# Kernel tuning notes

Measured on AMD Instinct MI355X. Metric: run time of the kernel, lower is better.

## Reference

```python
import jax, jax.numpy as jnp
import numpy as np

GH, GW, H, B, IN = 4, 2, 512, 8192, 1
FC_HID = H // 2
NC = GH * GW
BN_EPS = 1e-5


def setup_inputs() -> dict:
    key = jax.random.key(0)
    ks = jax.random.split(key, 20)
    def n(k, shape, s=1.0):
        return jax.random.normal(k, shape, dtype=jnp.float32) * s
    return {
        "x": n(ks[0], (B, GH, GW)),
        "h_ext": n(ks[1], (B, H), 0.1),
        "c_ext": n(ks[2], (B, H), 0.1),
        "grid_h": n(ks[3], (GH, GW, B, H), 0.1),
        "grid_c": n(ks[4], (GH, GW, B, H), 0.1),
        "Wh": n(ks[5], (NC, H, 3 * H), (3 * H) ** -0.5),
        "bh": n(ks[6], (NC, H), 0.01),
        "Wc": n(ks[7], (NC, H, 3 * H), (3 * H) ** -0.5),
        "bc": n(ks[8], (NC, H), 0.01),
        "W_ih": n(ks[9], (NC, 4 * H, IN), 1.0),
        "W_hh": n(ks[10], (NC, 4 * H, H), H ** -0.5),
        "b_ih": n(ks[11], (NC, 4 * H), 0.01),
        "b_hh": n(ks[12], (NC, 4 * H), 0.01),
        "W1": n(ks[13], (FC_HID, 2 * H), (2 * H) ** -0.5),
        "b1": n(ks[14], (FC_HID,), 0.01),
        "W2": n(ks[15], (1, FC_HID), FC_HID ** -0.5),
        "b2": n(ks[16], (1,), 0.01),
        "gamma": jnp.ones((1,), jnp.float32),
        "beta": jnp.zeros((1,), jnp.float32),
    }


def _lattice_forward(x, h_ext, c_ext, grid_h, grid_c, Wh, bh, Wc, bc,
                     W_ih, W_hh, b_ih, b_hh, W1, b1, W2, b2, gamma, beta):
    b = x.shape[0]
    zeros = jnp.zeros((b, H), x.dtype)
    # python lists over the small fixed 4x2 grid (strict left/up dependency)
    sh = [[grid_h[i, j] for j in range(GW)] for i in range(GH)]
    sc = [[grid_c[i, j] for j in range(GW)] for i in range(GH)]
    for i in range(GH):
        for j in range(GW):
            k = i * GW + j
            h_prev, c_prev = sh[i][j], sc[i][j]
            if i == 0 and j == 0:
                h_left, c_left = h_ext, c_ext
            elif j > 0:
                h_left, c_left = sh[i][j - 1], sc[i][j - 1]
            else:
                h_left, c_left = zeros, zeros
            if i > 0:
                h_up, c_up = sh[i - 1][j], sc[i - 1][j]
            else:
                h_up, c_up = zeros, zeros
            comb_h = jnp.concatenate([h_left, h_up, h_prev], axis=1)  # [B,3H]
            comb_c = jnp.concatenate([c_left, c_up, c_prev], axis=1)
            ph = comb_h @ Wh[k].T + bh[k]  # [B,H]
            pc = comb_c @ Wc[k].T + bc[k]
            xi = x[:, i, j][:, None]  # [B,1]
            gates = xi @ W_ih[k].T + b_ih[k] + ph @ W_hh[k].T + b_hh[k]  # [B,4H]
            ig, fg, gg, og = jnp.split(gates, 4, axis=1)
            c_new = jax.nn.sigmoid(fg) * pc + jax.nn.sigmoid(ig) * jnp.tanh(gg)
            h_new = jax.nn.sigmoid(og) * jnp.tanh(c_new)
            sh[i][j], sc[i][j] = h_new, c_new
    final_h = sh[-1][-1] + h_ext
    final_c = sc[-1][-1] + c_ext
    final = jnp.concatenate([final_h, final_c], axis=1)  # [B,2H]
    hid = jax.nn.relu(final @ W1.T + b1)
    out = hid @ W2.T + b2  # [B,1]
    # BatchNorm1d in training mode: biased batch stats over the batch dim
    mu = jnp.mean(out, axis=0, keepdims=True)
    var = jnp.mean((out - mu) ** 2, axis=0, keepdims=True)
    out = gamma * (out - mu) * jax.lax.rsqrt(var + BN_EPS) + beta
    out = jax.nn.sigmoid(out)
    new_gh = jnp.stack([jnp.stack(row) for row in sh])  # [GH,GW,B,H]
    new_gc = jnp.stack([jnp.stack(row) for row in sc])
    return out, final_h, final_c, new_gh, new_gc


def reference(x, h_ext, c_ext, grid_h, grid_c, Wh, bh, Wc, bc,
              W_ih, W_hh, b_ih, b_hh, W1, b1, W2, b2, gamma, beta):
    return _lattice_forward(x, h_ext, c_ext, grid_h, grid_c, Wh, bh, Wc, bc,
                            W_ih, W_hh, b_ih, b_hh, W1, b1, W2, b2, gamma, beta)
```

## Files before the change

kernel.cpp:

```cpp
#include <hip/hip_runtime.h>
#include <stdint.h>

#define B_SZ 8192
#define H_SZ 512
static const size_t BH = (size_t)B_SZ * H_SZ;

typedef short bfrag8 __attribute__((ext_vector_type(8)));
typedef float f32x4 __attribute__((ext_vector_type(4)));

__device__ __forceinline__ unsigned short f2bf(float f) {
  union { float f; uint32_t u; } c; c.f = f;
  uint32_t u = c.u;
  uint32_t r = (u + 0x7FFFu + ((u >> 16) & 1u)) >> 16;
  return (unsigned short)r;
}
__device__ __forceinline__ float bf2f(unsigned short u) {
  union { uint32_t u; float f; } c; c.u = ((uint32_t)u) << 16;
  return c.f;
}
__device__ __forceinline__ float sigm(float x) { return 1.0f / (1.0f + __expf(-x)); }
__device__ __forceinline__ float tanh_fast(float x) {
  float cx = fminf(fmaxf(x, -15.0f), 15.0f);
  float e = __expf(2.0f * cx);
  return (e - 1.0f) / (e + 1.0f);
}

__device__ __forceinline__ void gload16(const void* g, void* l) {
  __builtin_amdgcn_global_load_lds(
      (const __attribute__((address_space(1))) void*)g,
      (__attribute__((address_space(3))) void*)l, 16, 0, 0);
}

__device__ __forceinline__ void xcd_swizzle(int& bx, int& by, int& bz) {
  int nx = gridDim.x, ny = gridDim.y, nz = gridDim.z;
  int nwg = nx * ny * nz;
  int id = blockIdx.x + nx * (blockIdx.y + ny * blockIdx.z);
  int q = nwg >> 3, r = nwg & 7;
  int xcd = id & 7, lin = id >> 3;
  int swz = (xcd < r ? xcd * (q + 1) : r * (q + 1) + (xcd - r) * q) + lin;
  bx = swz % nx; swz /= nx;
  by = swz % ny; bz = swz / ny;
}

struct PJob {
  const unsigned short* A[3];
  int co[3];
  int nseg, relu;
  const unsigned short* B;
  const float* bias;
  unsigned short* outBf;
};
struct PArgs {
  PJob j[8];
  int ldA, ldB, outStride;
};

__global__ __launch_bounds__(256, 2) void pgemm_k(PArgs pa) {
  __shared__ __align__(16) char lds[65536];
  int bx, by, bz;
  xcd_swizzle(bx, by, bz);
  const PJob jb = pa.j[bz];
  const int tid = threadIdx.x;
  const int lane = tid & 63;
  const int wv = tid >> 6;
  const int wr = wv >> 1, wc = wv & 1;
  const int m0 = by * 128;
  const int ldA = pa.ldA;

  int rowA[4], cg[4];
  const char* browPtr[4];
#pragma unroll
  for (int q = 0; q < 4; ++q) {
    int cl = q * 256 + tid;
    int row = cl >> 3, cs = cl & 7;
    cg[q] = cs ^ (row & 7);
    rowA[q] = row;
    browPtr[q] = (const char*)jb.B + (size_t)(bx * 128 + row) * pa.ldB * 2;
  }

  f32x4 acc[4][4];
#pragma unroll
  for (int a = 0; a < 4; ++a)
#pragma unroll
    for (int b = 0; b < 4; ++b) acc[a][b] = f32x4{0.f, 0.f, 0.f, 0.f};

  const int nt = jb.nseg * 8;

  auto stagef = [&](int t, int buf) {
    int s = t >> 3, k0 = (t & 7) << 6;
    const char* Abase = (const char*)jb.A[s];
    int coB = jb.co[s] * 2;
    char* base = lds + buf * 32768;
#pragma unroll
    for (int q = 0; q < 4; ++q)
      gload16(Abase + ((size_t)(m0 + rowA[q]) * ldA + k0) * 2 + cg[q] * 16,
              base + (q * 256 + tid) * 16);
#pragma unroll
    for (int q = 0; q < 4; ++q)
      gload16(browPtr[q] + coB + k0 * 2 + cg[q] * 16,
              base + 16384 + (q * 256 + tid) * 16);
  };

  stagef(0, 0);
  int cur = 0;
  for (int t = 0; t < nt; ++t) {
    if (t + 1 < nt) {
      stagef(t + 1, cur ^ 1);
      asm volatile("s_waitcnt vmcnt(8)" ::: "memory");
    } else {
      asm volatile("s_waitcnt vmcnt(0)" ::: "memory");
    }
    __builtin_amdgcn_s_barrier();
    asm volatile("" ::: "memory");
    const char* As = lds + cur * 32768;
    const char* Bs = As + 16384;
    __builtin_amdgcn_s_setprio(1);
#pragma unroll
    for (int ks = 0; ks < 2; ++ks) {
      bfrag8 af[4], bfr[4];
#pragma unroll
      for (int mf = 0; mf < 4; ++mf) {
        int row = wr * 64 + mf * 16 + (lane & 15);
        af[mf] = *(const bfrag8*)(As + row * 128 +
                                  ((ks * 4 + (lane >> 4)) ^ (row & 7)) * 16);
      }
#pragma unroll
      for (int nf = 0; nf < 4; ++nf) {
        int row = wc * 64 + nf * 16 + (lane & 15);
        bfr[nf] = *(const bfrag8*)(Bs + row * 128 +
                                   ((ks * 4 + (lane >> 4)) ^ (row & 7)) * 16);
      }
#pragma unroll
      for (int mf = 0; mf < 4; ++mf)
#pragma unroll
        for (int nf = 0; nf < 4; ++nf)
          acc[mf][nf] = __builtin_amdgcn_mfma_f32_16x16x32_bf16(
              af[mf], bfr[nf], acc[mf][nf], 0, 0, 0);
    }
    __builtin_amdgcn_s_setprio(0);
    asm volatile("" ::: "memory");
    __builtin_amdgcn_s_barrier();
    asm volatile("" ::: "memory");
    cur ^= 1;
  }

  const int c4 = lane & 15;
  const int r4 = lane >> 4;
  const int n0 = bx * 128;
#pragma unroll
  for (int nf = 0; nf < 4; ++nf) {
    int colg = n0 + wc * 64 + nf * 16 + c4;
    float bv = jb.bias[colg];
#pragma unroll
    for (int mf = 0; mf < 4; ++mf)
#pragma unroll
      for (int r = 0; r < 4; ++r) {
        int rowg = m0 + wr * 64 + mf * 16 + r4 * 4 + r;
        size_t o = (size_t)rowg * pa.outStride + colg;
        float v = acc[mf][nf][r] + bv;
        if (jb.relu) v = fmaxf(v, 0.0f);
        jb.outBf[o] = f2bf(v);
      }
  }
}

struct GJob {
  const unsigned short* ph;
  const unsigned short* Whh;
  const unsigned short* pc;
  float* gh; float* gc;
  unsigned short* nh; unsigned short* nc;
  int cell, last;
};
struct GArgs {
  GJob j[2];
  const float* x;
  const float* W_ih; const float* b_ih; const float* b_hh;
  const float* h_ext; const float* c_ext;
  float* fh; float* fc;
  unsigned short* finalB;
};

__global__ __launch_bounds__(256, 2) void gates_k(GArgs ga) {
  __shared__ __align__(16) char lds[65536];
  int bx, by, bz;
  xcd_swizzle(bx, by, bz);
  const GJob jb = ga.j[bz];
  const int tid = threadIdx.x;
  const int lane = tid & 63;
  const int wv = tid >> 6;
  const int wr = wv >> 1, wc = wv & 1;
  const int m0 = by * 128;

  int rowA[4], cg[4];
  const char* browPtr[4];
#pragma unroll
  for (int q = 0; q < 4; ++q) {
    int cl = q * 256 + tid;
    int row = cl >> 3, cs = cl & 7;
    cg[q] = cs ^ (row & 7);
    rowA[q] = row;
    int gate = (row >> 4) & 3;
    int hh = bx * 32 + ((row >> 6) << 4) + (row & 15);
    browPtr[q] = (const char*)jb.Whh + (size_t)(gate * 512 + hh) * 512 * 2;
  }

  f32x4 acc[4][4];
#pragma unroll
  for (int a = 0; a < 4; ++a)
#pragma unroll
    for (int b = 0; b < 4; ++b) acc[a][b] = f32x4{0.f, 0.f, 0.f, 0.f};

  auto stagef = [&](int t, int buf) {
    int k0 = t << 6;
    char* base = lds + buf * 32768;
#pragma unroll
    for (int q = 0; q < 4; ++q)
      gload16((const char*)jb.ph + ((size_t)(m0 + rowA[q]) * 512 + k0) * 2 + cg[q] * 16,
              base + (q * 256 + tid) * 16);
#pragma unroll
    for (int q = 0; q < 4; ++q)
      gload16(browPtr[q] + k0 * 2 + cg[q] * 16,
              base + 16384 + (q * 256 + tid) * 16);
  };

  stagef(0, 0);
  int cur = 0;
  for (int t = 0; t < 8; ++t) {
    if (t + 1 < 8) {
      stagef(t + 1, cur ^ 1);
      asm volatile("s_waitcnt vmcnt(8)" ::: "memory");
    } else {
      asm volatile("s_waitcnt vmcnt(0)" ::: "memory");
    }
    __builtin_amdgcn_s_barrier();
    asm volatile("" ::: "memory");
    const char* As = lds + cur * 32768;
    const char* Bs = As + 16384;
    __builtin_amdgcn_s_setprio(1);
#pragma unroll
    for (int ks = 0; ks < 2; ++ks) {
      bfrag8 af[4], bfr[4];
#pragma unroll
      for (int mf = 0; mf < 4; ++mf) {
        int row = wr * 64 + mf * 16 + (lane & 15);
        af[mf] = *(const bfrag8*)(As + row * 128 +
                                  ((ks * 4 + (lane >> 4)) ^ (row & 7)) * 16);
      }
#pragma unroll
      for (int nf = 0; nf < 4; ++nf) {
        int row = wc * 64 + nf * 16 + (lane & 15);
        bfr[nf] = *(const bfrag8*)(Bs + row * 128 +
                                   ((ks * 4 + (lane >> 4)) ^ (row & 7)) * 16);
      }
#pragma unroll
      for (int mf = 0; mf < 4; ++mf)
#pragma unroll
        for (int nf = 0; nf < 4; ++nf)
          acc[mf][nf] = __builtin_amdgcn_mfma_f32_16x16x32_bf16(
              af[mf], bfr[nf], acc[mf][nf], 0, 0, 0);
    }
    __builtin_amdgcn_s_setprio(0);
    asm volatile("" ::: "memory");
    __builtin_amdgcn_s_barrier();
    asm volatile("" ::: "memory");
    cur ^= 1;
  }

  const int c4 = lane & 15;
  const int r4 = lane >> 4;
  int hcol = bx * 32 + wc * 16 + c4;
  const float* Wih = ga.W_ih + jb.cell * 2048;
  const float* bih = ga.b_ih + jb.cell * 2048;
  const float* bhh = ga.b_hh + jb.cell * 2048;
  float wih[4], gb[4];
#pragma unroll
  for (int q = 0; q < 4; ++q) {
    wih[q] = Wih[q * 512 + hcol];
    gb[q] = bih[q * 512 + hcol] + bhh[q * 512 + hcol];
  }
#pragma unroll
  for (int mf = 0; mf < 4; ++mf)
#pragma unroll
    for (int r = 0; r < 4; ++r) {
      int b = m0 + wr * 64 + mf * 16 + r4 * 4 + r;
      float xi = ga.x[b * 8 + jb.cell];
      float vi = acc[mf][0][r] + xi * wih[0] + gb[0];
      float vf = acc[mf][1][r] + xi * wih[1] + gb[1];
      float vg = acc[mf][2][r] + xi * wih[2] + gb[2];
      float vo = acc[mf][3][r] + xi * wih[3] + gb[3];
      size_t o = (size_t)b * 512 + hcol;
      float pcv = bf2f(jb.pc[o]);
      float cn = sigm(vf) * pcv + sigm(vi) * tanh_fast(vg);
      float hn = sigm(vo) * tanh_fast(cn);
      jb.gh[o] = hn;
      jb.gc[o] = cn;
      jb.nh[o] = f2bf(hn);
      jb.nc[o] = f2bf(cn);
      if (jb.last) {
        float fh = hn + ga.h_ext[o];
        float fc = cn + ga.c_ext[o];
        ga.fh[o] = fh;
        ga.fc[o] = fc;
        ga.finalB[(size_t)b * 1024 + hcol] = f2bf(fh);
        ga.finalB[(size_t)b * 1024 + 512 + hcol] = f2bf(fc);
      }
    }
}

struct CvtArgs {
  const float4* s[8];
  uint2* d[8];
  long start[9];
};
__global__ __launch_bounds__(256) void convert_many(CvtArgs ca) {
  long total = ca.start[8];
  long stride = (long)gridDim.x * blockDim.x;
  for (long idx = (long)blockIdx.x * blockDim.x + threadIdx.x; idx < total;
       idx += stride) {
    int jb = 0;
#pragma unroll
    for (int q = 1; q < 8; ++q) jb += (idx >= ca.start[q]) ? 1 : 0;
    long local = idx - ca.start[jb];
    float4 v = ca.s[jb][local];
    uint2 o;
    o.x = (uint32_t)f2bf(v.x) | ((uint32_t)f2bf(v.y) << 16);
    o.y = (uint32_t)f2bf(v.z) | ((uint32_t)f2bf(v.w) << 16);
    ca.d[jb][local] = o;
  }
}

__global__ __launch_bounds__(256)
void fc2_kernel(const unsigned short* hid, const float* W2, const float* b2,
                float* outlin) {
  int row = blockIdx.x * 4 + (threadIdx.x >> 6);
  int lane = threadIdx.x & 63;
  uint2 hv = ((const uint2*)(hid + (size_t)row * 256))[lane];
  float4 wv = ((const float4*)W2)[lane];
  float s = bf2f((unsigned short)(hv.x & 0xffffu)) * wv.x +
            bf2f((unsigned short)(hv.x >> 16)) * wv.y +
            bf2f((unsigned short)(hv.y & 0xffffu)) * wv.z +
            bf2f((unsigned short)(hv.y >> 16)) * wv.w;
#pragma unroll
  for (int o = 32; o > 0; o >>= 1) s += __shfl_down(s, o);
  if (lane == 0) outlin[row] = s + b2[0];
}

__global__ __launch_bounds__(1024)
void bn_kernel(const float* outlin, const float* gamma, const float* beta,
               float* out) {
  __shared__ float sred[16], sred2[16];
  __shared__ float smu, srs;
  float s = 0.f, s2 = 0.f;
  for (int i = threadIdx.x; i < 8192; i += 1024) {
    float v = outlin[i];
    s += v; s2 += v * v;
  }
#pragma unroll
  for (int o = 32; o > 0; o >>= 1) { s += __shfl_down(s, o); s2 += __shfl_down(s2, o); }
  if ((threadIdx.x & 63) == 0) { sred[threadIdx.x >> 6] = s; sred2[threadIdx.x >> 6] = s2; }
  __syncthreads();
  if (threadIdx.x == 0) {
    float S = 0.f, S2 = 0.f;
    for (int q = 0; q < 16; ++q) { S += sred[q]; S2 += sred2[q]; }
    float mu = S * (1.0f / 8192.0f);
    float var = S2 * (1.0f / 8192.0f) - mu * mu;
    smu = mu; srs = rsqrtf(var + 1e-5f);
  }
  __syncthreads();
  float gm = gamma[0], bt = beta[0];
  for (int i = threadIdx.x; i < 8192; i += 1024) {
    float v = (outlin[i] - smu) * srs * gm + bt;
    out[i] = sigm(v);
  }
}

extern "C" void kernel_launch(void* const* d_in, const int* in_sizes, int n_in,
                              void* d_out, int out_size, void* d_ws, size_t ws_size,
                              hipStream_t stream) {
  const float* x      = (const float*)d_in[0];
  const float* h_ext  = (const float*)d_in[1];
  const float* c_ext  = (const float*)d_in[2];
  const float* grid_h = (const float*)d_in[3];
  const float* grid_c = (const float*)d_in[4];
  const float* Wh     = (const float*)d_in[5];
  const float* bh     = (const float*)d_in[6];
  const float* Wc     = (const float*)d_in[7];
  const float* bc     = (const float*)d_in[8];
  const float* W_ih   = (const float*)d_in[9];
  const float* W_hh   = (const float*)d_in[10];
  const float* b_ih   = (const float*)d_in[11];
  const float* b_hh   = (const float*)d_in[12];
  const float* W1     = (const float*)d_in[13];
  const float* b1     = (const float*)d_in[14];
  const float* W2     = (const float*)d_in[15];
  const float* b2     = (const float*)d_in[16];
  const float* gamma  = (const float*)d_in[17];
  const float* beta   = (const float*)d_in[18];

  float* out = (float*)d_out;
  float* fh_out = out + 8192;
  float* fc_out = fh_out + BH;
  float* gh_out = fc_out + BH;
  float* gc_out = gh_out + 8 * BH;

  char* ws = (char*)d_ws;
  size_t off = 0;
  auto alloc = [&](size_t bytes) {
    char* p = ws + off;
    off = (off + bytes + 255) & ~(size_t)255;
    return p;
  };
  unsigned short* whB   = (unsigned short*)alloc(8ull * 512 * 1536 * 2);
  unsigned short* wcB   = (unsigned short*)alloc(8ull * 512 * 1536 * 2);
  unsigned short* whhB  = (unsigned short*)alloc(8ull * 2048 * 512 * 2);
  unsigned short* w1B   = (unsigned short*)alloc(256ull * 1024 * 2);
  unsigned short* hextB = (unsigned short*)alloc(BH * 2);
  unsigned short* cextB = (unsigned short*)alloc(BH * 2);
  unsigned short* prevH = (unsigned short*)alloc(8 * BH * 2);
  unsigned short* prevC = (unsigned short*)alloc(8 * BH * 2);
  unsigned short* newH  = (unsigned short*)alloc(8 * BH * 2);
  unsigned short* newC  = (unsigned short*)alloc(8 * BH * 2);
  unsigned short* pcB   = (unsigned short*)alloc(8 * BH * 2);
  unsigned short* phB   = (unsigned short*)alloc(8 * BH * 2);
  unsigned short* finalB = (unsigned short*)alloc((size_t)B_SZ * 1024 * 2);
  unsigned short* hidB   = (unsigned short*)alloc((size_t)B_SZ * 256 * 2);
  float*          outlin = (float*)alloc((size_t)B_SZ * 4);

  {
    CvtArgs ca;
    long n4[8] = {
        8L * 512 * 1536 / 4, 8L * 512 * 1536 / 4, 8L * 2048 * 512 / 4,
        256L * 1024 / 4,     (long)BH / 4,        (long)BH / 4,
        8L * (long)BH / 4,   8L * (long)BH / 4};
    const float* srcs[8] = {Wh, Wc, W_hh, W1, h_ext, c_ext, grid_h, grid_c};
    unsigned short* dsts[8] = {whB, wcB, whhB, w1B, hextB, cextB, prevH, prevC};
    ca.start[0] = 0;
    for (int q = 0; q < 8; ++q) {
      ca.s[q] = (const float4*)srcs[q];
      ca.d[q] = (uint2*)dsts[q];
      ca.start[q + 1] = ca.start[q] + n4[q];
    }
    convert_many<<<2048, 256, 0, stream>>>(ca);
  }

  auto launch_p = [&](const int* cells, int n) {
    PArgs pa = {};
    pa.ldA = 512; pa.ldB = 1536; pa.outStride = 512;
    for (int q = 0; q < n; ++q) {
      int k = cells[q];
      int i = k >> 1, jj = k & 1;
      PJob& jh = pa.j[2 * q];
      PJob& jc = pa.j[2 * q + 1];
      jh = PJob{}; jc = PJob{};
      int ns = 0;
      if (k == 0) {
        jh.A[ns] = hextB; jc.A[ns] = cextB; jh.co[ns] = 0; jc.co[ns] = 0; ns++;
      } else if (jj > 0) {
        jh.A[ns] = newH + (size_t)(k - 1) * BH;
        jc.A[ns] = newC + (size_t)(k - 1) * BH;
        jh.co[ns] = 0; jc.co[ns] = 0; ns++;
      }
      if (i > 0) {
        jh.A[ns] = newH + (size_t)(k - 2) * BH;
        jc.A[ns] = newC + (size_t)(k - 2) * BH;
        jh.co[ns] = 512; jc.co[ns] = 512; ns++;
      }
      jh.A[ns] = prevH + (size_t)k * BH;
      jc.A[ns] = prevC + (size_t)k * BH;
      jh.co[ns] = 1024; jc.co[ns] = 1024; ns++;
      jh.nseg = ns; jc.nseg = ns;
      jh.B = whB + (size_t)k * 512 * 1536; jh.bias = bh + k * 512;
      jc.B = wcB + (size_t)k * 512 * 1536; jc.bias = bc + k * 512;
      jh.outBf = phB + (size_t)k * BH;
      jc.outBf = pcB + (size_t)k * BH;
    }
    pgemm_k<<<dim3(4, 64, 2 * n), 256, 0, stream>>>(pa);
  };

  auto launch_gates = [&](const int* cells, int n) {
    GArgs ga = {};
    ga.x = x; ga.W_ih = W_ih; ga.b_ih = b_ih; ga.b_hh = b_hh;
    ga.h_ext = h_ext; ga.c_ext = c_ext;
    ga.fh = fh_out; ga.fc = fc_out; ga.finalB = finalB;
    for (int q = 0; q < n; ++q) {
      int k = cells[q];
      GJob& j = ga.j[q];
      j.ph = phB + (size_t)k * BH;
      j.Whh = whhB + (size_t)k * 2048 * 512;
      j.pc = pcB + (size_t)k * BH;
      j.gh = gh_out + (size_t)k * BH;
      j.gc = gc_out + (size_t)k * BH;
      j.nh = newH + (size_t)k * BH;
      j.nc = newC + (size_t)k * BH;
      j.cell = k; j.last = (k == 7);
    }
    gates_k<<<dim3(16, 64, n), 256, 0, stream>>>(ga);
  };

  const int diags[5][2] = {{0, -1}, {1, 2}, {3, 4}, {5, 6}, {7, -1}};
  const int dn[5] = {1, 2, 2, 2, 1};
  for (int d = 0; d < 5; ++d) {
    launch_p(diags[d], dn[d]);
    launch_gates(diags[d], dn[d]);
  }

  {
    PArgs pa = {};
    pa.ldA = 1024; pa.ldB = 1024; pa.outStride = 256;
    PJob& j = pa.j[0];
    j = PJob{};
    j.A[0] = finalB; j.co[0] = 0;
    j.A[1] = finalB + 512; j.co[1] = 512;
    j.nseg = 2; j.relu = 1;
    j.B = w1B; j.bias = b1; j.outBf = hidB;
    pgemm_k<<<dim3(2, 64, 1), 256, 0, stream>>>(pa);
  }

  fc2_kernel<<<2048, 256, 0, stream>>>(hidB, W2, b2, outlin);
  bn_kernel<<<1, 1024, 0, stream>>>(outlin, gamma, beta, out);
}
```

Before: 751.2 us.

## Read fp32 activations directly in projection GEMM, drop bf16 state copies

The projection GEMM gains a template path that loads fp32 A operands (h_ext, c_ext, grid state, new cell outputs) and converts them to bf16 in registers before storing to LDS. This removes the up-front conversion of the grid state and external state to bf16, and the extra bf16 copies of new h and c written by the gates kernel. In exchange, the GEMM drops its double-buffered async pipeline for a single-buffered loop with __syncthreads, uses half the LDS, and raises launch bounds to 4 blocks per CU. A operand traffic per tile doubles because fp32 is read instead of bf16.

```diff
diff --git a/kernel.cpp b/kernel.cpp
--- a/kernel.cpp
+++ b/kernel.cpp
@@ -2,8 +2,7 @@
 #include <stdint.h>
 
 #define B_SZ 8192
-#define H_SZ 512
-static const size_t BH = (size_t)B_SZ * H_SZ;
+static const size_t BH = (size_t)B_SZ * 512;
 
 typedef short bfrag8 __attribute__((ext_vector_type(8)));
 typedef float f32x4 __attribute__((ext_vector_type(4)));
@@ -17,6 +16,11 @@
 __device__ __forceinline__ float bf2f(unsigned short u) {
   union { uint32_t u; float f; } c; c.u = ((uint32_t)u) << 16;
   return c.f;
+}
+__device__ __forceinline__ uint32_t pk2(float a, float b) {
+  uint32_t r;
+  asm("v_cvt_pk_bf16_f32 %0, %1, %2" : "=v"(r) : "v"(a), "v"(b));
+  return r;
 }
 __device__ __forceinline__ float sigm(float x) { return 1.0f / (1.0f + __expf(-x)); }
 __device__ __forceinline__ float tanh_fast(float x) {
@@ -43,20 +47,23 @@
 }
 
 struct PJob {
-  const unsigned short* A[3];
+  const void* A[3];
   int co[3];
   int nseg, relu;
   const unsigned short* B;
   const float* bias;
   unsigned short* outBf;
+  unsigned short* outBf2;
 };
 struct PArgs {
   PJob j[8];
   int ldA, ldB, outStride;
 };
 
-__global__ __launch_bounds__(256, 2) void pgemm_k(PArgs pa) {
-  __shared__ __align__(16) char lds[65536];
+template <int AF32>
+__global__ __launch_bounds__(256, 4) void pgemm_k(PArgs pa) {
+  __shared__ __align__(16) char As[16384];
+  __shared__ __align__(16) char Bs[16384];
   int bx, by, bz;
   xcd_swizzle(bx, by, bz);
   const PJob jb = pa.j[bz];
@@ -84,64 +91,60 @@
 #pragma unroll
     for (int b = 0; b < 4; ++b) acc[a][b] = f32x4{0.f, 0.f, 0.f, 0.f};
 
-  const int nt = jb.nseg * 8;
-
-  auto stagef = [&](int t, int buf) {
-    int s = t >> 3, k0 = (t & 7) << 6;
-    const char* Abase = (const char*)jb.A[s];
-    int coB = jb.co[s] * 2;
-    char* base = lds + buf * 32768;
-#pragma unroll
-    for (int q = 0; q < 4; ++q)
-      gload16(Abase + ((size_t)(m0 + rowA[q]) * ldA + k0) * 2 + cg[q] * 16,
-              base + (q * 256 + tid) * 16);
-#pragma unroll
-    for (int q = 0; q < 4; ++q)
-      gload16(browPtr[q] + coB + k0 * 2 + cg[q] * 16,
-              base + 16384 + (q * 256 + tid) * 16);
-  };
-
-  stagef(0, 0);
-  int cur = 0;
-  for (int t = 0; t < nt; ++t) {
-    if (t + 1 < nt) {
-      stagef(t + 1, cur ^ 1);
-      asm volatile("s_waitcnt vmcnt(8)" ::: "memory");
-    } else {
-      asm volatile("s_waitcnt vmcnt(0)" ::: "memory");
-    }
-    __builtin_amdgcn_s_barrier();
-    asm volatile("" ::: "memory");
-    const char* As = lds + cur * 32768;
-    const char* Bs = As + 16384;
-    __builtin_amdgcn_s_setprio(1);
-#pragma unroll
-    for (int ks = 0; ks < 2; ++ks) {
-      bfrag8 af[4], bfr[4];
-#pragma unroll
-      for (int mf = 0; mf < 4; ++mf) {
-        int row = wr * 64 + mf * 16 + (lane & 15);
-        af[mf] = *(const bfrag8*)(As + row * 128 +
-                                  ((ks * 4 + (lane >> 4)) ^ (row & 7)) * 16);
-      }
-#pragma unroll
-      for (int nf = 0; nf < 4; ++nf) {
-        int row = wc * 64 + nf * 16 + (lane & 15);
-        bfr[nf] = *(const bfrag8*)(Bs + row * 128 +
-                                   ((ks * 4 + (lane >> 4)) ^ (row & 7)) * 16);
-      }
-#pragma unroll
-      for (int mf = 0; mf < 4; ++mf)
-#pragma unroll
-        for (int nf = 0; nf < 4; ++nf)
-          acc[mf][nf] = __builtin_amdgcn_mfma_f32_16x16x32_bf16(
-              af[mf], bfr[nf], acc[mf][nf], 0, 0, 0);
-    }
-    __builtin_amdgcn_s_setprio(0);
-    asm volatile("" ::: "memory");
-    __builtin_amdgcn_s_barrier();
-    asm volatile("" ::: "memory");
-    cur ^= 1;
+  for (int s = 0; s < jb.nseg; ++s) {
+    const int coB = jb.co[s] * 2;
+    for (int k0 = 0; k0 < 512; k0 += 64) {
+#pragma unroll
+      for (int q = 0; q < 4; ++q)
+        gload16(browPtr[q] + coB + k0 * 2 + cg[q] * 16,
+                Bs + (q * 256 + tid) * 16);
+      if (AF32) {
+        const float* Ab = (const float*)jb.A[s];
+#pragma unroll
+        for (int q = 0; q < 4; ++q) {
+          const float4* p = (const float4*)(Ab + (size_t)(m0 + rowA[q]) * ldA +
+                                            k0 + cg[q] * 8);
+          float4 a0 = p[0];
+          float4 a1 = p[1];
+          uint4 w;
+          w.x = pk2(a0.x, a0.y);
+          w.y = pk2(a0.z, a0.w);
+          w.z = pk2(a1.x, a1.y);
+          w.w = pk2(a1.z, a1.w);
+          *(uint4*)(As + (q * 256 + tid) * 16) = w;
+        }
+      } else {
+        const char* Ab = (const char*)jb.A[s];
+#pragma unroll
+        for (int q = 0; q < 4; ++q)
+          gload16(Ab + ((size_t)(m0 + rowA[q]) * ldA + k0) * 2 + cg[q] * 16,
+                  As + (q * 256 + tid) * 16);
+      }
+      __syncthreads();
+#pragma unroll
+      for (int ks = 0; ks < 2; ++ks) {
+        bfrag8 af[4], bfr[4];
+#pragma unroll
+        for (int mf = 0; mf < 4; ++mf) {
+          int row = wr * 64 + mf * 16 + (lane & 15);
+          af[mf] = *(const bfrag8*)(As + row * 128 +
+                                    ((ks * 4 + (lane >> 4)) ^ (row & 7)) * 16);
+        }
+#pragma unroll
+        for (int nf = 0; nf < 4; ++nf) {
+          int row = wc * 64 + nf * 16 + (lane & 15);
+          bfr[nf] = *(const bfrag8*)(Bs + row * 128 +
+                                     ((ks * 4 + (lane >> 4)) ^ (row & 7)) * 16);
+        }
+#pragma unroll
+        for (int mf = 0; mf < 4; ++mf)
+#pragma unroll
+          for (int nf = 0; nf < 4; ++nf)
+            acc[mf][nf] = __builtin_amdgcn_mfma_f32_16x16x32_bf16(
+                af[mf], bfr[nf], acc[mf][nf], 0, 0, 0);
+      }
+      __syncthreads();
+    }
   }
 
   const int c4 = lane & 15;
@@ -169,7 +172,6 @@
   const unsigned short* Whh;
   const unsigned short* pc;
   float* gh; float* gc;
-  unsigned short* nh; unsigned short* nc;
   int cell, last;
 };
 struct GArgs {
@@ -295,8 +297,6 @@
       float hn = sigm(vo) * tanh_fast(cn);
       jb.gh[o] = hn;
       jb.gc[o] = cn;
-      jb.nh[o] = f2bf(hn);
-      jb.nc[o] = f2bf(cn);
       if (jb.last) {
         float fh = hn + ga.h_ext[o];
         float fc = cn + ga.c_ext[o];
@@ -415,12 +415,6 @@
   unsigned short* wcB   = (unsigned short*)alloc(8ull * 512 * 1536 * 2);
   unsigned short* whhB  = (unsigned short*)alloc(8ull * 2048 * 512 * 2);
   unsigned short* w1B   = (unsigned short*)alloc(256ull * 1024 * 2);
-  unsigned short* hextB = (unsigned short*)alloc(BH * 2);
-  unsigned short* cextB = (unsigned short*)alloc(BH * 2);
-  unsigned short* prevH = (unsigned short*)alloc(8 * BH * 2);
-  unsigned short* prevC = (unsigned short*)alloc(8 * BH * 2);
-  unsigned short* newH  = (unsigned short*)alloc(8 * BH * 2);
-  unsigned short* newC  = (unsigned short*)alloc(8 * BH * 2);
   unsigned short* pcB   = (unsigned short*)alloc(8 * BH * 2);
   unsigned short* phB   = (unsigned short*)alloc(8 * BH * 2);
   unsigned short* finalB = (unsigned short*)alloc((size_t)B_SZ * 1024 * 2);
@@ -429,17 +423,16 @@
 
   {
     CvtArgs ca;
-    long n4[8] = {
-        8L * 512 * 1536 / 4, 8L * 512 * 1536 / 4, 8L * 2048 * 512 / 4,
-        256L * 1024 / 4,     (long)BH / 4,        (long)BH / 4,
-        8L * (long)BH / 4,   8L * (long)BH / 4};
-    const float* srcs[8] = {Wh, Wc, W_hh, W1, h_ext, c_ext, grid_h, grid_c};
-    unsigned short* dsts[8] = {whB, wcB, whhB, w1B, hextB, cextB, prevH, prevC};
+    long n4[4] = {8L * 512 * 1536 / 4, 8L * 512 * 1536 / 4,
+                  8L * 2048 * 512 / 4, 256L * 1024 / 4};
+    const float* srcs[4] = {Wh, Wc, W_hh, W1};
+    unsigned short* dsts[4] = {whB, wcB, whhB, w1B};
     ca.start[0] = 0;
     for (int q = 0; q < 8; ++q) {
-      ca.s[q] = (const float4*)srcs[q];
-      ca.d[q] = (uint2*)dsts[q];
-      ca.start[q + 1] = ca.start[q] + n4[q];
+      int qq = q < 4 ? q : 3;
+      ca.s[q] = (const float4*)srcs[qq];
+      ca.d[q] = (uint2*)dsts[qq];
+      ca.start[q + 1] = ca.start[q] + (q < 4 ? n4[q] : 0);
     }
     convert_many<<<2048, 256, 0, stream>>>(ca);
   }
@@ -455,19 +448,20 @@
       jh = PJob{}; jc = PJob{};
       int ns = 0;
       if (k == 0) {
-        jh.A[ns] = hextB; jc.A[ns] = cextB; jh.co[ns] = 0; jc.co[ns] = 0; ns++;
+        jh.A[ns] = h_ext; jc.A[ns] = c_ext;
+        jh.co[ns] = 0; jc.co[ns] = 0; ns++;
       } else if (jj > 0) {
-        jh.A[ns] = newH + (size_t)(k - 1) * BH;
-        jc.A[ns] = newC + (size_t)(k - 1) * BH;
+        jh.A[ns] = gh_out + (size_t)(k - 1) * BH;
+        jc.A[ns] = gc_out + (size_t)(k - 1) * BH;
         jh.co[ns] = 0; jc.co[ns] = 0; ns++;
       }
       if (i > 0) {
-        jh.A[ns] = newH + (size_t)(k - 2) * BH;
-        jc.A[ns] = newC + (size_t)(k - 2) * BH;
+        jh.A[ns] = gh_out + (size_t)(k - 2) * BH;
+        jc.A[ns] = gc_out + (size_t)(k - 2) * BH;
         jh.co[ns] = 512; jc.co[ns] = 512; ns++;
       }
-      jh.A[ns] = prevH + (size_t)k * BH;
-      jc.A[ns] = prevC + (size_t)k * BH;
+      jh.A[ns] = grid_h + (size_t)k * BH;
+      jc.A[ns] = grid_c + (size_t)k * BH;
       jh.co[ns] = 1024; jc.co[ns] = 1024; ns++;
       jh.nseg = ns; jc.nseg = ns;
       jh.B = whB + (size_t)k * 512 * 1536; jh.bias = bh + k * 512;
@@ -475,7 +469,7 @@
       jh.outBf = phB + (size_t)k * BH;
       jc.outBf = pcB + (size_t)k * BH;
     }
-    pgemm_k<<<dim3(4, 64, 2 * n), 256, 0, stream>>>(pa);
+    pgemm_k<1><<<dim3(4, 64, 2 * n), 256, 0, stream>>>(pa);
   };
 
   auto launch_gates = [&](const int* cells, int n) {
@@ -491,8 +485,6 @@
       j.pc = pcB + (size_t)k * BH;
       j.gh = gh_out + (size_t)k * BH;
       j.gc = gc_out + (size_t)k * BH;
-      j.nh = newH + (size_t)k * BH;
-      j.nc = newC + (size_t)k * BH;
       j.cell = k; j.last = (k == 7);
     }
     gates_k<<<dim3(16, 64, n), 256, 0, stream>>>(ga);
@@ -514,7 +506,7 @@
     j.A[1] = finalB + 512; j.co[1] = 512;
     j.nseg = 2; j.relu = 1;
     j.B = w1B; j.bias = b1; j.outBf = hidB;
-    pgemm_k<<<dim3(2, 64, 1), 256, 0, stream>>>(pa);
+    pgemm_k<0><<<dim3(2, 64, 1), 256, 0, stream>>>(pa);
   }
 
   fc2_kernel<<<2048, 256, 0, stream>>>(hidB, W2, b2, outlin);
```

New measurement: 752.4 us. About the same (+0.2%).
